# Kernel tuning notes

Measured on AMD Instinct MI355X. Metric: run time of the kernel, lower is better.

Reference implementation:

```python
import jax, jax.numpy as jnp
import numpy as np

L, B, S, C, H, V = 12, 2, 1024, 768, 12, 50257
D = C // H
FF = 4 * C
SCALE = 1.0 / float(np.sqrt(D))


def setup_inputs() -> dict:
    key = jax.random.key(0)
    ks = jax.random.split(key, 10)
    s = 0.02  # GPT-2 init std
    return {
        "idx": jax.random.randint(ks[0], (B, S), 0, V),
        "targets": jax.random.randint(ks[1], (B, S), 0, V),
        "wte": jax.random.normal(ks[2], (V, C), jnp.float32) * s,
        "wpe": jax.random.normal(ks[3], (S, C), jnp.float32) * s,
        "ln1_w": jnp.ones((L, C), jnp.float32),
        "ln1_b": jnp.zeros((L, C), jnp.float32),
        "qkv_w": jax.random.normal(ks[4], (L, C, 3 * C), jnp.float32) * s,
        "qkv_b": jnp.zeros((L, 3 * C), jnp.float32),
        "proj_w": jax.random.normal(ks[5], (L, C, C), jnp.float32) * s,
        "proj_b": jnp.zeros((L, C), jnp.float32),
        "ln2_w": jnp.ones((L, C), jnp.float32),
        "ln2_b": jnp.zeros((L, C), jnp.float32),
        "fc_w": jax.random.normal(ks[6], (L, C, FF), jnp.float32) * s,
        "fc_b": jnp.zeros((L, FF), jnp.float32),
        "fc2_w": jax.random.normal(ks[7], (L, FF, C), jnp.float32) * s,
        "fc2_b": jnp.zeros((L, C), jnp.float32),
        "lnf_w": jnp.ones((C,), jnp.float32),
        "lnf_b": jnp.zeros((C,), jnp.float32),
    }


def _ln(x, w, b):
    m = jnp.mean(x, axis=-1, keepdims=True)
    v = jnp.mean(jnp.square(x - m), axis=-1, keepdims=True)
    return (x - m) * jax.lax.rsqrt(v + 1e-5) * w + b


def _gpt(wte, wpe, ln1_w, ln1_b, qkv_w, qkv_b, proj_w, proj_b,
         ln2_w, ln2_b, fc_w, fc_b, fc2_w, fc2_b, lnf_w, lnf_b, idx, targets):
    h = wte[idx] + wpe[jnp.arange(S)]  # [B,S,C]
    causal = jnp.tril(jnp.ones((S, S), bool))

    def block(h, p):
        l1w, l1b, qw, qb, pw, pb, l2w, l2b, fw, fb, gw, gb = p
        x = _ln(h, l1w, l1b)
        q, k, v = jnp.split(x @ qw + qb, 3, axis=-1)  # each [B,S,C]
        heads = lambda t: t.reshape(B, S, H, D).transpose(0, 2, 1, 3)  # [B,H,S,D]
        q, k, v = heads(q), heads(k), heads(v)
        scores = jnp.einsum('bhsd,bhtd->bhst', q, k) * SCALE
        scores = jnp.where(causal, scores, -jnp.inf)
        att = jax.nn.softmax(scores, axis=-1)
        o = jnp.einsum('bhst,bhtd->bhsd', att, v)
        o = o.transpose(0, 2, 1, 3).reshape(B, S, C)
        h = h + o @ pw + pb
        x = _ln(h, l2w, l2b)
        h = h + jax.nn.gelu(x @ fw + fb, approximate=True) @ gw + gb
        return h, None

    h, _ = jax.lax.scan(block, h, (ln1_w, ln1_b, qkv_w, qkv_b, proj_w, proj_b,
                                   ln2_w, ln2_b, fc_w, fc_b, fc2_w, fc2_b))
    logits = _ln(h, lnf_w, lnf_b) @ wte.T  # tied lm_head, [B,S,V]
    logp = jax.nn.log_softmax(logits, axis=-1)
    loss = -jnp.mean(jnp.take_along_axis(logp, targets[..., None], axis=-1))
    return logits, loss


def reference(idx, targets, wte, wpe, ln1_w, ln1_b, qkv_w, qkv_b, proj_w, proj_b,
              ln2_w, ln2_b, fc_w, fc_b, fc2_w, fc2_b, lnf_w, lnf_b):
    return _gpt(wte, wpe, ln1_w, ln1_b, qkv_w, qkv_b, proj_w, proj_b,
                ln2_w, ln2_b, fc_w, fc_b, fc2_w, fc2_b, lnf_w, lnf_b, idx, targets)
```

## Files before the change

kernel.cpp:

```cpp
#include <hip/hip_runtime.h>
#include <hip/hip_bf16.h>
#include <cstdint>
#include <cstddef>

constexpr int LNUM = 12;
constexpr int BB   = 2;
constexpr int SS   = 1024;
constexpr int CC   = 768;
constexpr int HH   = 12;
constexpr int DD   = 64;
constexpr int FFD  = 3072;
constexpr int VV   = 50257;
constexpr int VPAD = 50304;
constexpr int NBX  = VPAD / 128;
constexpr int MM   = BB * SS;

typedef unsigned short u16;
typedef short     s16x8 __attribute__((ext_vector_type(8)));
typedef float     f32x4 __attribute__((ext_vector_type(4)));
typedef u16       u16x4 __attribute__((ext_vector_type(4)));
typedef u16       u16x8 __attribute__((ext_vector_type(8)));

__device__ __forceinline__ float bf2f(u16 v) {
    return __uint_as_float(((unsigned)v) << 16);
}
__device__ __forceinline__ u16 f2bf(float f) {
    unsigned u = __float_as_uint(f);
    return (u16)((u + 0x7fffu + ((u >> 16) & 1u)) >> 16);
}


__global__ __launch_bounds__(256) void wte_conv_kernel(const float* __restrict__ wte,
                                                       u16* __restrict__ out) {
    size_t i4 = ((size_t)blockIdx.x * 256 + threadIdx.x) * 4;
    if (i4 >= (size_t)VPAD * CC) return;
    size_t r = i4 / CC;
    u16x4 o;
    if (r < (size_t)VV) {
        const float4 v = *(const float4*)&wte[i4];
        o[0] = f2bf(v.x); o[1] = f2bf(v.y); o[2] = f2bf(v.z); o[3] = f2bf(v.w);
    } else {
        o[0] = o[1] = o[2] = o[3] = 0;
    }
    *(u16x4*)&out[i4] = o;
}

__global__ __launch_bounds__(256) void transpose_conv_kernel(const float* __restrict__ in,
                                                             u16* __restrict__ out,
                                                             int R, int Cn) {
    __shared__ float tile[32][33];
    const float* inp = in + (size_t)blockIdx.z * R * Cn;
    u16* outp = out + (size_t)blockIdx.z * R * Cn;
    int c  = blockIdx.x * 32 + threadIdx.x;
    int r0 = blockIdx.y * 32;
#pragma unroll
    for (int i = 0; i < 4; ++i) {
        int r = r0 + threadIdx.y + i * 8;
        tile[threadIdx.y + i * 8][threadIdx.x] = inp[(size_t)r * Cn + c];
    }
    __syncthreads();
    int oc = r0 + threadIdx.x;
#pragma unroll
    for (int i = 0; i < 4; ++i) {
        int orow = blockIdx.x * 32 + threadIdx.y + i * 8;
        outp[(size_t)orow * R + oc] = f2bf(tile[threadIdx.x][threadIdx.y + i * 8]);
    }
}

__global__ __launch_bounds__(256) void embed_kernel(const int* __restrict__ idx,
                                                    const float* __restrict__ wte,
                                                    const float* __restrict__ wpe,
                                                    float* __restrict__ h) {
    int row = blockIdx.x;
    int s   = row & (SS - 1);
    int tok = idx[row];
    const float* we = wte + (size_t)tok * CC;
    const float* pe = wpe + (size_t)s * CC;
    float* hr = h + (size_t)row * CC;
    for (int c = threadIdx.x; c < CC; c += 256) hr[c] = we[c] + pe[c];
}

__global__ __launch_bounds__(256) void ln_kernel(const float* __restrict__ h,
                                                 const float* __restrict__ w,
                                                 const float* __restrict__ b,
                                                 u16* __restrict__ x) {
    int row = blockIdx.x, tid = threadIdx.x;
    const float* hr = h + (size_t)row * CC;
    float v0 = hr[tid], v1 = hr[tid + 256], v2 = hr[tid + 512];
    float s  = v0 + v1 + v2;
    float s2 = v0 * v0 + v1 * v1 + v2 * v2;
#pragma unroll
    for (int off = 32; off; off >>= 1) {
        s  += __shfl_xor(s, off);
        s2 += __shfl_xor(s2, off);
    }
    __shared__ float rs[4], rs2[4], stat[2];
    int wid = tid >> 6;
    if ((tid & 63) == 0) { rs[wid] = s; rs2[wid] = s2; }
    __syncthreads();
    if (tid == 0) {
        float ts  = rs[0] + rs[1] + rs[2] + rs[3];
        float ts2 = rs2[0] + rs2[1] + rs2[2] + rs2[3];
        float mean = ts * (1.0f / CC);
        float var  = ts2 * (1.0f / CC) - mean * mean;
        stat[0] = mean;
        stat[1] = rsqrtf(var + 1e-5f);
    }
    __syncthreads();
    float mean = stat[0], rstd = stat[1];
    size_t base = (size_t)row * CC;
    x[base + tid]       = f2bf((v0 - mean) * rstd * w[tid]       + b[tid]);
    x[base + tid + 256] = f2bf((v1 - mean) * rstd * w[tid + 256] + b[tid + 256]);
    x[base + tid + 512] = f2bf((v2 - mean) * rstd * w[tid + 512] + b[tid + 512]);
}

template <int BM, int BN, int EPI>
__global__ __launch_bounds__(256)
void gemm_bt_kernel(const u16* __restrict__ A, const u16* __restrict__ Bt,
                    const float* __restrict__ bias, float* __restrict__ outf,
                    u16* __restrict__ outb, int K, long long ldo,
                    float* __restrict__ partM, float* __restrict__ partS) {
    constexpr int MR  = BM / 32, NR = BN / 32;
    constexpr int ACH = BM * 64 / (256 * 8);
    constexpr int BCH = BN * 64 / (256 * 8);
    __shared__ u16 As[BM * 64];
    __shared__ u16 Bs[BN * 64];
    const int tid  = threadIdx.x;
    const int lane = tid & 63;
    const int wid  = tid >> 6;
    const int l15  = lane & 15;
    const int lq   = lane >> 4;
    const int wm   = wid & 1;
    const int wn   = wid >> 1;
    const int rx   = l15 & 7;

    const int gx = gridDim.x, gy = gridDim.y;
    const int nwg = gx * gy;
    const int pos = blockIdx.y * gx + blockIdx.x;
    const int qc  = nwg >> 3, rc = nwg & 7;
    const int xcd = pos & 7, cidx = pos >> 3;
    const int wgid = (xcd < rc ? xcd * (qc + 1) : rc * (qc + 1) + (xcd - rc) * qc) + cidx;
    const int bx = wgid / gy, by = wgid % gy;
    const int bm0 = by * BM, bn0 = bx * BN;

    f32x4 acc[MR][NR];
#pragma unroll
    for (int m = 0; m < MR; ++m)
#pragma unroll
        for (int n = 0; n < NR; ++n) acc[m][n] = (f32x4){0.f, 0.f, 0.f, 0.f};

    u16x8 areg[ACH], breg[BCH];
    auto ldreg = [&](int kt) {
#pragma unroll
        for (int it = 0; it < ACH; ++it) {
            int g = it * 256 + tid, r = g >> 3, c = ((g & 7) ^ (r & 7)) * 8;
            areg[it] = *(const u16x8*)&A[(size_t)(bm0 + r) * (size_t)K + kt + c];
        }
#pragma unroll
        for (int it = 0; it < BCH; ++it) {
            int g = it * 256 + tid, r = g >> 3, c = ((g & 7) ^ (r & 7)) * 8;
            breg[it] = *(const u16x8*)&Bt[(size_t)(bn0 + r) * (size_t)K + kt + c];
        }
    };
    auto wlds = [&]() {
#pragma unroll
        for (int it = 0; it < ACH; ++it) *(u16x8*)&As[(it * 256 + tid) * 8] = areg[it];
#pragma unroll
        for (int it = 0; it < BCH; ++it) *(u16x8*)&Bs[(it * 256 + tid) * 8] = breg[it];
    };
    auto compute = [&]() {
#pragma unroll
        for (int ks = 0; ks < 2; ++ks) {
            s16x8 af[MR], bfr[NR];
#pragma unroll
            for (int m = 0; m < MR; ++m) {
                int row = wm * (BM / 2) + m * 16 + l15;
                af[m] = *(const s16x8*)&As[row * 64 + (((ks * 4 + lq) ^ rx) * 8)];
            }
#pragma unroll
            for (int n = 0; n < NR; ++n) {
                int row = wn * (BN / 2) + n * 16 + l15;
                bfr[n] = *(const s16x8*)&Bs[row * 64 + (((ks * 4 + lq) ^ rx) * 8)];
            }
#pragma unroll
            for (int m = 0; m < MR; ++m)
#pragma unroll
                for (int n = 0; n < NR; ++n)
                    acc[m][n] = __builtin_amdgcn_mfma_f32_16x16x32_bf16(af[m], bfr[n], acc[m][n], 0, 0, 0);
        }
    };

    const int nk = K >> 6;
    ldreg(0);
    for (int t = 0; t < nk; ++t) {
        __syncthreads();
        wlds();
        __syncthreads();
        if (t + 1 < nk) ldreg((t + 1) << 6);
        compute();
    }

#pragma unroll
    for (int m = 0; m < MR; ++m) {
#pragma unroll
        for (int n = 0; n < NR; ++n) {
#pragma unroll
            for (int r = 0; r < 4; ++r) {
                int row = bm0 + wm * (BM / 2) + m * 16 + lq * 4 + r;
                int col = bn0 + wn * (BN / 2) + n * 16 + l15;
                float v = acc[m][n][r];
                if (EPI != 3) v += bias[col];
                if (EPI == 1) {
                    float z = 0.7978845608028654f * (v + 0.044715f * v * v * v);
                    v = v / (1.0f + __expf(-2.0f * z));
                }
                if (EPI == 0 || EPI == 1) {
                    outb[(size_t)row * ldo + col] = f2bf(v);
                } else if (EPI == 2) {
                    outf[(size_t)row * ldo + col] += v;
                } else {
                    if (col < VV) outf[(size_t)row * ldo + col] = v;
                }
            }
        }
    }

    if constexpr (EPI == 3) {
        __shared__ float redM[2][BM], redS[2][BM];
#pragma unroll
        for (int m = 0; m < MR; ++m) {
#pragma unroll
            for (int r = 0; r < 4; ++r) {
                float mx = -3.0e38f;
#pragma unroll
                for (int n = 0; n < NR; ++n) {
                    int colg = bn0 + wn * (BN / 2) + n * 16 + l15;
                    float v = (colg < VV) ? acc[m][n][r] : -3.0e38f;
                    mx = fmaxf(mx, v);
                }
#pragma unroll
                for (int off = 1; off < 16; off <<= 1) mx = fmaxf(mx, __shfl_xor(mx, off));
                float sm = 0.f;
#pragma unroll
                for (int n = 0; n < NR; ++n) {
                    int colg = bn0 + wn * (BN / 2) + n * 16 + l15;
                    if (colg < VV) sm += __expf(acc[m][n][r] - mx);
                }
#pragma unroll
                for (int off = 1; off < 16; off <<= 1) sm += __shfl_xor(sm, off);
                if (l15 == 0) {
                    int rl = wm * (BM / 2) + m * 16 + lq * 4 + r;
                    redM[wn][rl] = mx;
                    redS[wn][rl] = sm;
                }
            }
        }
        __syncthreads();
        if (tid < BM) {
            float m0 = redM[0][tid], m1 = redM[1][tid];
            float M = fmaxf(m0, m1);
            float S = redS[0][tid] * __expf(m0 - M) + redS[1][tid] * __expf(m1 - M);
            size_t rowg = (size_t)(bm0 + tid);
            partM[rowg * NBX + bx] = M;
            partS[rowg * NBX + bx] = S;
        }
    }
}

__global__ __launch_bounds__(256) void vtrans_kernel(const u16* __restrict__ qkv,
                                                     u16* __restrict__ vT) {
    __shared__ u16 T[64 * 64];
    const int tid = threadIdx.x;
    const int t0  = blockIdx.x * 64;
    const int bh  = blockIdx.y;
    const int b   = bh / HH, hh = bh % HH;
    const u16* vp = qkv + (size_t)b * SS * (3 * CC) + 2 * CC + hh * DD;
#pragma unroll
    for (int it = 0; it < 2; ++it) {
        int g = it * 256 + tid;
        int t = g >> 3, dg = g & 7;
        u16x8 v = *(const u16x8*)&vp[(size_t)(t0 + t) * (3 * CC) + dg * 8];
        *(u16x8*)&T[(t * 8 + (dg ^ (t & 7))) * 8] = v;
    }
    __syncthreads();
    u16* op = vT + (size_t)bh * DD * SS + t0;
#pragma unroll
    for (int it = 0; it < 2; ++it) {
        int g = it * 256 + tid;
        int d = g >> 3, tc = g & 7;
        u16x8 o;
#pragma unroll
        for (int e = 0; e < 8; ++e) {
            int t = tc * 8 + e;
            o[e] = T[(t * 8 + ((d >> 3) ^ (t & 7))) * 8 + (d & 7)];
        }
        *(u16x8*)&op[(size_t)d * SS + tc * 8] = o;
    }
}

__global__ __launch_bounds__(256) void attn_mfma3_kernel(const u16* __restrict__ qkv,
                                                         const u16* __restrict__ vT,
                                                         u16* __restrict__ o) {
    constexpr int PADC = 72;
    __shared__ u16 Ks[64][PADC];
    __shared__ u16 Vs[64][PADC];
    __shared__ u16 Ps[4][16][PADC];

    const int tid = threadIdx.x, lane = tid & 63, wid = tid >> 6;
    const int l15 = lane & 15, lq = lane >> 4;
    const int pos = blockIdx.x;
    const int j   = 15 - pos / 24;
    const int bh  = pos % 24;
    const int b   = bh / HH, hh = bh % HH;
    const int q0  = j * 64;

    const size_t base = (size_t)b * SS * (3 * CC);
    const u16* kp = qkv + base + CC + hh * DD;
    const u16* vp = vT + (size_t)bh * DD * SS;

    s16x8 qf[2];
    {
        const u16* qr = qkv + base + hh * DD + (size_t)(q0 + wid * 16 + l15) * (3 * CC);
        qf[0] = *(const s16x8*)&qr[lq * 8];
        qf[1] = *(const s16x8*)&qr[32 + lq * 8];
    }

    float m[4], lsum[4];
    f32x4 acc_o[4];
#pragma unroll
    for (int r = 0; r < 4; ++r) { m[r] = -3.0e38f; lsum[r] = 0.f; }
#pragma unroll
    for (int nd = 0; nd < 4; ++nd) acc_o[nd] = (f32x4){0.f, 0.f, 0.f, 0.f};

    const int sr = tid >> 3, sc = (tid & 7) * 8;
    const int sr1 = sr + 32;
    u16x8 kreg[2], vreg[2];
    auto ldkv = [&](int t0) {
        kreg[0] = *(const u16x8*)&kp[(size_t)(t0 + sr) * (3 * CC) + sc];
        vreg[0] = *(const u16x8*)&vp[(size_t)sr * SS + t0 + sc];
        kreg[1] = *(const u16x8*)&kp[(size_t)(t0 + sr1) * (3 * CC) + sc];
        vreg[1] = *(const u16x8*)&vp[(size_t)sr1 * SS + t0 + sc];
    };

    ldkv(0);
    for (int tt = 0; tt <= j; ++tt) {
        __syncthreads();
        *(u16x8*)&Ks[sr][sc]  = kreg[0];
        *(u16x8*)&Vs[sr][sc]  = vreg[0];
        *(u16x8*)&Ks[sr1][sc] = kreg[1];
        *(u16x8*)&Vs[sr1][sc] = vreg[1];
        __syncthreads();
        if (tt < j) ldkv((tt + 1) * 64);

        f32x4 sc4[4];
#pragma unroll
        for (int n = 0; n < 4; ++n) sc4[n] = (f32x4){0.f, 0.f, 0.f, 0.f};
#pragma unroll
        for (int ks = 0; ks < 2; ++ks) {
#pragma unroll
            for (int n = 0; n < 4; ++n) {
                s16x8 kb = *(const s16x8*)&Ks[n * 16 + l15][ks * 32 + lq * 8];
                sc4[n] = __builtin_amdgcn_mfma_f32_16x16x32_bf16(qf[ks], kb, sc4[n], 0, 0, 0);
            }
        }

        const int t0 = tt * 64;
        if (tt == j) {
#pragma unroll
            for (int n = 0; n < 4; ++n) {
                int colg = t0 + n * 16 + l15;
#pragma unroll
                for (int r = 0; r < 4; ++r) {
                    int rowg = q0 + wid * 16 + lq * 4 + r;
                    float sv = sc4[n][r] * 0.125f;
                    sc4[n][r] = (colg <= rowg) ? sv : -3.0e38f;
                }
            }
        } else {
#pragma unroll
            for (int n = 0; n < 4; ++n)
#pragma unroll
                for (int r = 0; r < 4; ++r) sc4[n][r] *= 0.125f;
        }

        float mt[4];
#pragma unroll
        for (int r = 0; r < 4; ++r)
            mt[r] = fmaxf(fmaxf(sc4[0][r], sc4[1][r]), fmaxf(sc4[2][r], sc4[3][r]));
#pragma unroll
        for (int off = 1; off < 16; off <<= 1)
#pragma unroll
            for (int r = 0; r < 4; ++r) mt[r] = fmaxf(mt[r], __shfl_xor(mt[r], off));
        float rs[4];
#pragma unroll
        for (int r = 0; r < 4; ++r) {
            float mn  = fmaxf(m[r], mt[r]);
            float scl = __expf(m[r] - mn);
            m[r] = mn;
            float ps = 0.f;
#pragma unroll
            for (int n = 0; n < 4; ++n) {
                float p = __expf(sc4[n][r] - mn);
                sc4[n][r] = p;
                ps += p;
            }
            rs[r] = ps;
            lsum[r] *= scl;
#pragma unroll
            for (int nd = 0; nd < 4; ++nd) acc_o[nd][r] *= scl;
        }
#pragma unroll
        for (int off = 1; off < 16; off <<= 1)
#pragma unroll
            for (int r = 0; r < 4; ++r) rs[r] += __shfl_xor(rs[r], off);
#pragma unroll
        for (int r = 0; r < 4; ++r) lsum[r] += rs[r];

#pragma unroll
        for (int n = 0; n < 4; ++n)
#pragma unroll
            for (int r = 0; r < 4; ++r)
                Ps[wid][lq * 4 + r][n * 16 + l15] = f2bf(sc4[n][r]);

#pragma unroll
        for (int ks = 0; ks < 2; ++ks) {
            s16x8 pa = *(const s16x8*)&Ps[wid][l15][ks * 32 + lq * 8];
#pragma unroll
            for (int nd = 0; nd < 4; ++nd) {
                s16x8 vb = *(const s16x8*)&Vs[nd * 16 + l15][ks * 32 + lq * 8];
                acc_o[nd] = __builtin_amdgcn_mfma_f32_16x16x32_bf16(pa, vb, acc_o[nd], 0, 0, 0);
            }
        }
    }

#pragma unroll
    for (int r = 0; r < 4; ++r) {
        float inv = 1.f / lsum[r];
        int rowg = q0 + wid * 16 + lq * 4 + r;
        u16* orow = o + ((size_t)b * SS + rowg) * CC + hh * DD;
#pragma unroll
        for (int nd = 0; nd < 4; ++nd)
            orow[nd * 16 + l15] = f2bf(acc_o[nd][r] * inv);
    }
}

__global__ __launch_bounds__(256) void lse_kernel(const float* __restrict__ partM,
                                                  const float* __restrict__ partS,
                                                  const float* __restrict__ logits,
                                                  const int* __restrict__ tgt,
                                                  float* __restrict__ lossp) {
    int row = blockIdx.x, tid = threadIdx.x;
    float m = -3.0e38f, s = 0.f;
    for (int i = tid; i < NBX; i += 256) {
        float pm = partM[(size_t)row * NBX + i];
        float ps = partS[(size_t)row * NBX + i];
        float nm = fmaxf(m, pm);
        s = s * __expf(m - nm) + ps * __expf(pm - nm);
        m = nm;
    }
#pragma unroll
    for (int off = 32; off; off >>= 1) {
        float om = __shfl_xor(m, off), os = __shfl_xor(s, off);
        float nm = fmaxf(m, om);
        s = s * __expf(m - nm) + os * __expf(om - nm);
        m = nm;
    }
    __shared__ float rm[4], rsh[4];
    int wid = tid >> 6;
    if ((tid & 63) == 0) { rm[wid] = m; rsh[wid] = s; }
    __syncthreads();
    if (tid == 0) {
        float M = fmaxf(fmaxf(rm[0], rm[1]), fmaxf(rm[2], rm[3]));
        float S = rsh[0] * __expf(rm[0] - M) + rsh[1] * __expf(rm[1] - M) +
                  rsh[2] * __expf(rm[2] - M) + rsh[3] * __expf(rm[3] - M);
        float lse = M + __logf(S);
        lossp[row] = lse - logits[(size_t)row * VV + tgt[row]];
    }
}

__global__ __launch_bounds__(256) void loss_reduce_kernel(const float* __restrict__ lossp,
                                                          float* __restrict__ out) {
    int tid = threadIdx.x;
    float s = 0.f;
    for (int i = tid; i < MM; i += 256) s += lossp[i];
#pragma unroll
    for (int off = 32; off; off >>= 1) s += __shfl_xor(s, off);
    __shared__ float r[4];
    if ((tid & 63) == 0) r[tid >> 6] = s;
    __syncthreads();
    if (tid == 0) out[0] = (r[0] + r[1] + r[2] + r[3]) * (1.0f / MM);
}

extern "C" void kernel_launch(void* const* d_in, const int* in_sizes, int n_in,
                              void* d_out, int out_size, void* d_ws, size_t ws_size,
                              hipStream_t stream) {
    const int*   idx     = (const int*)  d_in[0];
    const int*   targets = (const int*)  d_in[1];
    const float* wte     = (const float*)d_in[2];
    const float* wpe     = (const float*)d_in[3];
    const float* ln1w    = (const float*)d_in[4];
    const float* ln1b    = (const float*)d_in[5];
    const float* qkvw    = (const float*)d_in[6];
    const float* qkvbi   = (const float*)d_in[7];
    const float* projw   = (const float*)d_in[8];
    const float* projbi  = (const float*)d_in[9];
    const float* ln2w    = (const float*)d_in[10];
    const float* ln2b    = (const float*)d_in[11];
    const float* fcw     = (const float*)d_in[12];
    const float* fcbi    = (const float*)d_in[13];
    const float* fc2w    = (const float*)d_in[14];
    const float* fc2bi   = (const float*)d_in[15];
    const float* lnfw    = (const float*)d_in[16];
    const float* lnfb    = (const float*)d_in[17];
    float* logits = (float*)d_out;

    char* wsb = (char*)d_ws;
    size_t off = 0;
    auto alloc = [&](size_t n) -> char* {
        char* p = wsb + off;
        off = (off + n + 255) & ~(size_t)255;
        return p;
    };
    u16*   wteT  = (u16*)  alloc((size_t)VPAD * CC * 2);
    u16*   qkvT  = (u16*)  alloc((size_t)LNUM * 3 * CC * CC * 2);
    u16*   projT = (u16*)  alloc((size_t)LNUM * CC * CC * 2);
    u16*   fcT   = (u16*)  alloc((size_t)LNUM * FFD * CC * 2);
    u16*   fc2T  = (u16*)  alloc((size_t)LNUM * CC * FFD * 2);
    float* h     = (float*)alloc((size_t)MM * CC * 4);
    u16*   xb    = (u16*)  alloc((size_t)MM * CC * 2);
    u16*   qkvb  = (u16*)  alloc((size_t)MM * 3 * CC * 2);
    u16*   ob    = (u16*)  alloc((size_t)MM * CC * 2);
    u16*   gb    = (u16*)  alloc((size_t)MM * FFD * 2);
    u16*   vTb   = (u16*)  alloc((size_t)BB * HH * DD * SS * 2);
    float* lossp = (float*)alloc((size_t)MM * 4);
    float* partM = (float*)alloc((size_t)MM * NBX * 4);
    float* partS = (float*)alloc((size_t)MM * NBX * 4);

    {
        int blocks = (int)(((size_t)VPAD * CC / 4 + 255) / 256);
        wte_conv_kernel<<<blocks, 256, 0, stream>>>(wte, wteT);
    }
    transpose_conv_kernel<<<dim3(3 * CC / 32, CC / 32, LNUM), dim3(32, 8), 0, stream>>>(qkvw, qkvT, CC, 3 * CC);
    transpose_conv_kernel<<<dim3(CC / 32, CC / 32, LNUM),     dim3(32, 8), 0, stream>>>(projw, projT, CC, CC);
    transpose_conv_kernel<<<dim3(FFD / 32, CC / 32, LNUM),    dim3(32, 8), 0, stream>>>(fcw, fcT, CC, FFD);
    transpose_conv_kernel<<<dim3(CC / 32, FFD / 32, LNUM),    dim3(32, 8), 0, stream>>>(fc2w, fc2T, FFD, CC);

    embed_kernel<<<MM, 256, 0, stream>>>(idx, wte, wpe, h);

    for (int l = 0; l < LNUM; ++l) {
        const u16* qkvT_l  = qkvT  + (size_t)l * 3 * CC * CC;
        const u16* projT_l = projT + (size_t)l * CC * CC;
        const u16* fcT_l   = fcT   + (size_t)l * FFD * CC;
        const u16* fc2T_l  = fc2T  + (size_t)l * CC * FFD;

        ln_kernel<<<MM, 256, 0, stream>>>(h, ln1w + (size_t)l * CC, ln1b + (size_t)l * CC, xb);
        gemm_bt_kernel<128, 128, 0><<<dim3(3 * CC / 128, MM / 128), 256, 0, stream>>>(
            xb, qkvT_l, qkvbi + (size_t)l * 3 * CC, nullptr, qkvb, CC, 3 * CC, nullptr, nullptr);
        vtrans_kernel<<<dim3(SS / 64, BB * HH), 256, 0, stream>>>(qkvb, vTb);
        attn_mfma3_kernel<<<BB * HH * 16, 256, 0, stream>>>(qkvb, vTb, ob);
        gemm_bt_kernel<64, 64, 2><<<dim3(CC / 64, MM / 64), 256, 0, stream>>>(
            ob, projT_l, projbi + (size_t)l * CC, h, nullptr, CC, CC, nullptr, nullptr);
        ln_kernel<<<MM, 256, 0, stream>>>(h, ln2w + (size_t)l * CC, ln2b + (size_t)l * CC, xb);
        gemm_bt_kernel<128, 128, 1><<<dim3(FFD / 128, MM / 128), 256, 0, stream>>>(
            xb, fcT_l, fcbi + (size_t)l * FFD, nullptr, gb, CC, FFD, nullptr, nullptr);
        gemm_bt_kernel<64, 64, 2><<<dim3(CC / 64, MM / 64), 256, 0, stream>>>(
            gb, fc2T_l, fc2bi + (size_t)l * CC, h, nullptr, FFD, CC, nullptr, nullptr);
    }

    ln_kernel<<<MM, 256, 0, stream>>>(h, lnfw, lnfb, xb);
    gemm_bt_kernel<128, 128, 3><<<dim3(VPAD / 128, MM / 128), 256, 0, stream>>>(
        xb, wteT, nullptr, logits, nullptr, CC, VV, partM, partS);

    lse_kernel<<<MM, 256, 0, stream>>>(partM, partS, logits, targets, lossp);
    loss_reduce_kernel<<<1, 256, 0, stream>>>(lossp, logits + (size_t)MM * VV);
}
```

Measured before the change: 1.990 ms.

## Add BK template to GEMM, nontemporal logits stores, MFMA priority in attention

Makes the GEMM K-tile size a template parameter and uses BK=128 for the two 64x64 residual GEMMs (proj, fc2), halving their K-loop iterations and barriers, with a swizzle extended to 16 chunks per row. The lm_head epilogue now writes the large logits array with nontemporal stores to avoid polluting cache. The attention kernel raises wave priority around its MFMA blocks with s_setprio. These are three unrelated tweaks; larger LDS tiles may reduce occupancy for the 64x64 GEMMs.

```diff
diff --git a/kernel.cpp b/kernel.cpp
--- a/kernel.cpp
+++ b/kernel.cpp
@@ -114,17 +114,18 @@
     x[base + tid + 512] = f2bf((v2 - mean) * rstd * w[tid + 512] + b[tid + 512]);
 }
 
-template <int BM, int BN, int EPI>
+template <int BM, int BN, int BK, int EPI>
 __global__ __launch_bounds__(256)
 void gemm_bt_kernel(const u16* __restrict__ A, const u16* __restrict__ Bt,
                     const float* __restrict__ bias, float* __restrict__ outf,
                     u16* __restrict__ outb, int K, long long ldo,
                     float* __restrict__ partM, float* __restrict__ partS) {
     constexpr int MR  = BM / 32, NR = BN / 32;
-    constexpr int ACH = BM * 64 / (256 * 8);
-    constexpr int BCH = BN * 64 / (256 * 8);
-    __shared__ u16 As[BM * 64];
-    __shared__ u16 Bs[BN * 64];
+    constexpr int ACH = BM * BK / (256 * 8);
+    constexpr int BCH = BN * BK / (256 * 8);
+    constexpr int CPR = BK / 8;
+    __shared__ u16 As[BM * BK];
+    __shared__ u16 Bs[BN * BK];
     const int tid  = threadIdx.x;
     const int lane = tid & 63;
     const int wid  = tid >> 6;
@@ -153,12 +154,14 @@
     auto ldreg = [&](int kt) {
 #pragma unroll
         for (int it = 0; it < ACH; ++it) {
-            int g = it * 256 + tid, r = g >> 3, c = ((g & 7) ^ (r & 7)) * 8;
+            int g = it * 256 + tid, r = g / CPR, p = g % CPR;
+            int c = ((((p & 7) ^ (r & 7)) | (p & 8))) * 8;
             areg[it] = *(const u16x8*)&A[(size_t)(bm0 + r) * (size_t)K + kt + c];
         }
 #pragma unroll
         for (int it = 0; it < BCH; ++it) {
-            int g = it * 256 + tid, r = g >> 3, c = ((g & 7) ^ (r & 7)) * 8;
+            int g = it * 256 + tid, r = g / CPR, p = g % CPR;
+            int c = ((((p & 7) ^ (r & 7)) | (p & 8))) * 8;
             breg[it] = *(const u16x8*)&Bt[(size_t)(bn0 + r) * (size_t)K + kt + c];
         }
     };
@@ -170,17 +173,19 @@
     };
     auto compute = [&]() {
 #pragma unroll
-        for (int ks = 0; ks < 2; ++ks) {
+        for (int ks = 0; ks < BK / 32; ++ks) {
+            const int ck = ks * 4 + lq;
+            const int co = (((ck & 7) ^ rx) | (ck & 8)) * 8;
             s16x8 af[MR], bfr[NR];
 #pragma unroll
             for (int m = 0; m < MR; ++m) {
                 int row = wm * (BM / 2) + m * 16 + l15;
-                af[m] = *(const s16x8*)&As[row * 64 + (((ks * 4 + lq) ^ rx) * 8)];
+                af[m] = *(const s16x8*)&As[row * BK + co];
             }
 #pragma unroll
             for (int n = 0; n < NR; ++n) {
                 int row = wn * (BN / 2) + n * 16 + l15;
-                bfr[n] = *(const s16x8*)&Bs[row * 64 + (((ks * 4 + lq) ^ rx) * 8)];
+                bfr[n] = *(const s16x8*)&Bs[row * BK + co];
             }
 #pragma unroll
             for (int m = 0; m < MR; ++m)
@@ -190,13 +195,13 @@
         }
     };
 
-    const int nk = K >> 6;
+    const int nk = K / BK;
     ldreg(0);
     for (int t = 0; t < nk; ++t) {
         __syncthreads();
         wlds();
         __syncthreads();
-        if (t + 1 < nk) ldreg((t + 1) << 6);
+        if (t + 1 < nk) ldreg((t + 1) * BK);
         compute();
     }
 
@@ -219,7 +224,7 @@
                 } else if (EPI == 2) {
                     outf[(size_t)row * ldo + col] += v;
                 } else {
-                    if (col < VV) outf[(size_t)row * ldo + col] = v;
+                    if (col < VV) __builtin_nontemporal_store(v, &outf[(size_t)row * ldo + col]);
                 }
             }
         }
@@ -355,6 +360,7 @@
         f32x4 sc4[4];
 #pragma unroll
         for (int n = 0; n < 4; ++n) sc4[n] = (f32x4){0.f, 0.f, 0.f, 0.f};
+        __builtin_amdgcn_s_setprio(1);
 #pragma unroll
         for (int ks = 0; ks < 2; ++ks) {
 #pragma unroll
@@ -363,6 +369,7 @@
                 sc4[n] = __builtin_amdgcn_mfma_f32_16x16x32_bf16(qf[ks], kb, sc4[n], 0, 0, 0);
             }
         }
+        __builtin_amdgcn_s_setprio(0);
 
         const int t0 = tt * 64;
         if (tt == j) {
@@ -422,6 +429,7 @@
             for (int r = 0; r < 4; ++r)
                 Ps[wid][lq * 4 + r][n * 16 + l15] = f2bf(sc4[n][r]);
 
+        __builtin_amdgcn_s_setprio(1);
 #pragma unroll
         for (int ks = 0; ks < 2; ++ks) {
             s16x8 pa = *(const s16x8*)&Ps[wid][l15][ks * 32 + lq * 8];
@@ -431,6 +439,7 @@
                 acc_o[nd] = __builtin_amdgcn_mfma_f32_16x16x32_bf16(pa, vb, acc_o[nd], 0, 0, 0);
             }
         }
+        __builtin_amdgcn_s_setprio(0);
     }
 
 #pragma unroll
@@ -554,21 +563,21 @@
         const u16* fc2T_l  = fc2T  + (size_t)l * CC * FFD;
 
         ln_kernel<<<MM, 256, 0, stream>>>(h, ln1w + (size_t)l * CC, ln1b + (size_t)l * CC, xb);
-        gemm_bt_kernel<128, 128, 0><<<dim3(3 * CC / 128, MM / 128), 256, 0, stream>>>(
+        gemm_bt_kernel<128, 128, 64, 0><<<dim3(3 * CC / 128, MM / 128), 256, 0, stream>>>(
             xb, qkvT_l, qkvbi + (size_t)l * 3 * CC, nullptr, qkvb, CC, 3 * CC, nullptr, nullptr);
         vtrans_kernel<<<dim3(SS / 64, BB * HH), 256, 0, stream>>>(qkvb, vTb);
         attn_mfma3_kernel<<<BB * HH * 16, 256, 0, stream>>>(qkvb, vTb, ob);
-        gemm_bt_kernel<64, 64, 2><<<dim3(CC / 64, MM / 64), 256, 0, stream>>>(
+        gemm_bt_kernel<64, 64, 128, 2><<<dim3(CC / 64, MM / 64), 256, 0, stream>>>(
             ob, projT_l, projbi + (size_t)l * CC, h, nullptr, CC, CC, nullptr, nullptr);
         ln_kernel<<<MM, 256, 0, stream>>>(h, ln2w + (size_t)l * CC, ln2b + (size_t)l * CC, xb);
-        gemm_bt_kernel<128, 128, 1><<<dim3(FFD / 128, MM / 128), 256, 0, stream>>>(
+        gemm_bt_kernel<128, 128, 64, 1><<<dim3(FFD / 128, MM / 128), 256, 0, stream>>>(
             xb, fcT_l, fcbi + (size_t)l * FFD, nullptr, gb, CC, FFD, nullptr, nullptr);
-        gemm_bt_kernel<64, 64, 2><<<dim3(CC / 64, MM / 64), 256, 0, stream>>>(
+        gemm_bt_kernel<64, 64, 128, 2><<<dim3(CC / 64, MM / 64), 256, 0, stream>>>(
             gb, fc2T_l, fc2bi + (size_t)l * CC, h, nullptr, FFD, CC, nullptr, nullptr);
     }
 
     ln_kernel<<<MM, 256, 0, stream>>>(h, lnfw, lnfb, xb);
-    gemm_bt_kernel<128, 128, 3><<<dim3(VPAD / 128, MM / 128), 256, 0, stream>>>(
+    gemm_bt_kernel<128, 128, 64, 3><<<dim3(VPAD / 128, MM / 128), 256, 0, stream>>>(
         xb, wteT, nullptr, logits, nullptr, CC, VV, partM, partS);
 
     lse_kernel<<<MM, 256, 0, stream>>>(partM, partS, logits, targets, lossp);
```

After: 2.075 ms. +4.3%, slower.
